# Performance work log

Hardware: AMD Instinct MI355X
Metric: run time of the kernel (lower is better)

## Reference

```python
import jax, jax.numpy as jnp
import numpy as np
from jax import lax

B, H, W, C, NH = 16, 56, 56, 192, 6
L = H * W
DH = C // NH            # 32
HID = 4 * C             # 768
ETA = 1.0 / DH          # TTT inner-loop learning rate
EPS = 1e-5

# ---- RoPE rotation tables (deterministic buffer, shape (H, W, C//2)) ----
_kmax = C // 4
_theta = 1.0 / (10000.0 ** (np.arange(_kmax) / _kmax))
_ii, _jj = np.meshgrid(np.arange(H), np.arange(W), indexing='ij')
_ang = np.concatenate([_ii[..., None] * _theta, _jj[..., None] * _theta], axis=-1)  # (H,W,C/2)
_COS = jnp.asarray(np.cos(_ang), dtype=jnp.float32)
_SIN = jnp.asarray(np.sin(_ang), dtype=jnp.float32)


def layernorm(x, g, b):
    mu = jnp.mean(x, axis=-1, keepdims=True)
    var = jnp.mean(jnp.square(x - mu), axis=-1, keepdims=True)
    return (x - mu) * lax.rsqrt(var + EPS) * g + b


def dwconv3x3(x_blc, w, b):
    # x: (B, L, Ch) -> depthwise 3x3 conv over (H, W) -> (B, L, Ch)
    Ch = x_blc.shape[-1]
    xi = x_blc.reshape(B, H, W, Ch).transpose(0, 3, 1, 2)  # NCHW
    y = lax.conv_general_dilated(xi, w, (1, 1), 'SAME', feature_group_count=Ch,
                                 dimension_numbers=('NCHW', 'OIHW', 'NCHW'))
    y = y + b[None, :, None, None]
    return y.transpose(0, 2, 3, 1).reshape(B, L, Ch)


def rope(x):
    # x: (B, L, C); rotate complex pairs with 2D axial angles
    xr = x.reshape(B, H, W, C // 2, 2)
    re, im = xr[..., 0], xr[..., 1]
    o_re = _COS * re - _SIN * im
    o_im = _SIN * re + _COS * im
    return jnp.stack([o_re, o_im], axis=-1).reshape(B, L, C)


def ttt_attn(xn, qkv_w, qkv_b, W0, proj_w, proj_b):
    qkv = xn @ qkv_w.T + qkv_b                      # (B, L, 3C)
    q, k, v = jnp.split(qkv, 3, axis=-1)
    q = rope(q) * (DH ** -0.5)
    k = rope(k)

    def to_heads(t):  # (B,L,C) -> (L, B*NH, DH)
        return t.reshape(B, L, NH, DH).transpose(1, 0, 2, 3).reshape(L, B * NH, DH)
    qs, ks, vs = to_heads(q), to_heads(k), to_heads(v)

    Wst0 = jnp.broadcast_to(W0[None], (B, NH, DH, DH)).reshape(B * NH, DH, DH)

    def step(Wst, qkv_t):
        qt, kt, vt = qkv_t
        pred = jnp.einsum('bij,bj->bi', Wst, kt)
        Wn = Wst - ETA * (pred - vt)[:, :, None] * kt[:, None, :]
        ot = jnp.einsum('bij,bj->bi', Wn, qt)
        return Wn, ot

    _, out = lax.scan(step, Wst0, (qs, ks, vs))     # out: (L, B*NH, DH)
    out = out.reshape(L, B, NH, DH).transpose(1, 0, 2, 3).reshape(B, L, C)
    return out @ proj_w.T + proj_b


def setup_inputs() -> dict:
    key = jax.random.key(0)
    ks = jax.random.split(key, 12)
    s = 0.02
    return {
        'x': jax.random.normal(ks[0], (B, L, C), jnp.float32),
        'cpe_w': jax.random.normal(ks[1], (C, 1, 3, 3), jnp.float32) * s,
        'cpe_b': jnp.zeros((C,), jnp.float32),
        'n1_g': jnp.ones((C,), jnp.float32),
        'n1_b': jnp.zeros((C,), jnp.float32),
        'qkv_w': jax.random.normal(ks[2], (3 * C, C), jnp.float32) * s,
        'qkv_b': jnp.zeros((3 * C,), jnp.float32),
        'W0': jax.random.normal(ks[3], (NH, DH, DH), jnp.float32) * s,
        'proj_w': jax.random.normal(ks[4], (C, C), jnp.float32) * s,
        'proj_b': jnp.zeros((C,), jnp.float32),
        'n2_g': jnp.ones((C,), jnp.float32),
        'n2_b': jnp.zeros((C,), jnp.float32),
        'fc1_w': jax.random.normal(ks[5], (HID, C), jnp.float32) * s,
        'fc1_b': jnp.zeros((HID,), jnp.float32),
        'dwc_w': jax.random.normal(ks[6], (HID, 1, 3, 3), jnp.float32) * s,
        'dwc_b': jnp.zeros((HID,), jnp.float32),
        'fc2_w': jax.random.normal(ks[7], (C, HID), jnp.float32) * s,
        'fc2_b': jnp.zeros((C,), jnp.float32),
    }


def reference(x, cpe_w, cpe_b, n1_g, n1_b, qkv_w, qkv_b, W0, proj_w, proj_b,
              n2_g, n2_b, fc1_w, fc1_b, dwc_w, dwc_b, fc2_w, fc2_b):
    # CPE: conditional positional encoding (depthwise conv residual)
    x = x + dwconv3x3(x, cpe_w, cpe_b)
    # TTT attention branch
    x = x + ttt_attn(layernorm(x, n1_g, n1_b), qkv_w, qkv_b, W0, proj_w, proj_b)
    # MLP branch with depthwise conv
    h1 = jax.nn.gelu(layernorm(x, n2_g, n2_b) @ fc1_w.T + fc1_b, approximate=False)
    h1 = jax.nn.gelu(h1 + dwconv3x3(h1, dwc_w, dwc_b), approximate=False)
    x = x + (h1 @ fc2_w.T + fc2_b)
    return x
```

## Files before the change

### kernel.cpp

```cpp
#include <hip/hip_runtime.h>
#include <hip/hip_bf16.h>

#define Bc 16
#define Hc 56
#define Wcc 56
#define Cc 192
#define NHc 6
#define Lc 3136
#define DHc 32
#define HIDc 768
#define NHEAD 96
#define Sc 32
#define NCHUNK 98
#define NPAIR (NHEAD*NCHUNK)
#define ROWS (Bc*Lc)
#define GR2 (ROWS/2)
#define ETAc (1.0f/32.0f)

typedef unsigned short u16;
typedef unsigned int u32;
typedef __attribute__((ext_vector_type(8))) short bf16x8;
typedef __attribute__((ext_vector_type(4))) float f32x4;
typedef __attribute__((ext_vector_type(16))) float f32x16;

__device__ __forceinline__ float b2f(u16 v){ u32 u = ((u32)v)<<16; float f; __builtin_memcpy(&f,&u,4); return f; }
__device__ __forceinline__ u16 f2b(float f){ u32 u; __builtin_memcpy(&u,&f,4); u32 r = u + 0x7FFFu + ((u>>16)&1u); return (u16)(r>>16); }
__device__ __forceinline__ f32x16 zero16(){ f32x16 z = {0,0,0,0,0,0,0,0,0,0,0,0,0,0,0,0}; return z; }

__device__ __forceinline__ void make_bfrags(const f32x16& t, int hi, bf16x8& b1, bf16x8& b2){
  u32 P[8], S[8];
  #pragma unroll
  for (int q=0;q<4;q++){
    #pragma unroll
    for (int j=0;j<2;j++){
      u32 r; float lo = t[4*q+2*j], hv = t[4*q+2*j+1];
      asm("v_cvt_pk_bf16_f32 %0, %1, %2" : "=v"(r) : "v"(lo), "v"(hv));
      P[2*q+j] = r;
    }
  }
  #pragma unroll
  for (int i=0;i<8;i++) S[i] = (u32)__shfl_xor((int)P[i], 32);
  union { u32 u[4]; bf16x8 v; } f1, f2;
  if (hi==0){ f1.u[0]=P[0]; f1.u[1]=P[1]; f1.u[2]=S[0]; f1.u[3]=S[1];
              f2.u[0]=P[4]; f2.u[1]=P[5]; f2.u[2]=S[4]; f2.u[3]=S[5]; }
  else      { f1.u[0]=S[2]; f1.u[1]=S[3]; f1.u[2]=P[2]; f1.u[3]=P[3];
              f2.u[0]=S[6]; f2.u[1]=S[7]; f2.u[2]=P[6]; f2.u[3]=P[7]; }
  b1 = f1.v; b2 = f2.v;
}

__global__ __launch_bounds__(256) void prep_kernel(
    const float* __restrict__ qkvw, const float* __restrict__ projw,
    const float* __restrict__ fc1w, const float* __restrict__ fc2w,
    const float* __restrict__ dwcw, const float* __restrict__ cpew,
    u16* __restrict__ wbqkv, u16* __restrict__ wbproj, u16* __restrict__ wbfc1,
    u16* __restrict__ wbfc2, float* __restrict__ dwt9, float* __restrict__ cwt9){
  int i = blockIdx.x*256 + threadIdx.x;
  if (i < 110592) wbqkv[i] = f2b(qkvw[i]);
  else if (i < 147456){ int j=i-110592; wbproj[j] = f2b(projw[j]); }
  else if (i < 294912){ int j=i-147456; wbfc1[j] = f2b(fc1w[j]); }
  else if (i < 442368){ int j=i-294912; wbfc2[j] = f2b(fc2w[j]); }
  else if (i < 449280){ int j=i-442368; int ch=j/9, t=j-ch*9; dwt9[t*HIDc+ch] = dwcw[j]; }
  else if (i < 451008){ int j=i-449280; int ch=j/9, t=j-ch*9; cwt9[t*Cc+ch] = cpew[j]; }
}

__global__ __launch_bounds__(256) void rope_tab_kernel(float* __restrict__ ct, float* __restrict__ st){
  int i = blockIdx.x*256 + threadIdx.x;
  int l = i/96, p = i - l*96;
  int h = l/Wcc, w = l - h*Wcc;
  int kk = (p<48)? p : p-48;
  float th = powf(10000.f, -(float)kk/48.f);
  float ang = (float)((p<48)? h : w) * th;
  ct[i] = cosf(ang);
  st[i] = sinf(ang);
}

__global__ __launch_bounds__(192) void cpe_ln_kernel(const float* __restrict__ x, const float* __restrict__ cwt9,
                                                     const float* __restrict__ bs, const float* __restrict__ g,
                                                     const float* __restrict__ b,
                                                     u16* __restrict__ x1, u16* __restrict__ xn){
  __shared__ float ps[192], pq[192], smu[8], srs[8];
  int tid = threadIdx.x;
  int rl = tid/24, sub = tid - rl*24, ch0 = sub*8;
  int row = blockIdx.x*8 + rl;
  int l = row % Lc; int h = l/Wcc, w = l - h*Wcc;
  const float* xp = x + (size_t)row*Cc + ch0;
  float acc[8];
  { f32x4 b0 = *(const f32x4*)(bs+ch0), b1v = *(const f32x4*)(bs+ch0+4);
    acc[0]=b0[0];acc[1]=b0[1];acc[2]=b0[2];acc[3]=b0[3];
    acc[4]=b1v[0];acc[5]=b1v[1];acc[6]=b1v[2];acc[7]=b1v[3]; }
  #pragma unroll
  for (int kh=0;kh<3;kh++){
    int hh = h+kh-1; if (hh<0 || hh>=Hc) continue;
    #pragma unroll
    for (int kw=0;kw<3;kw++){
      int ww = w+kw-1; if (ww<0 || ww>=Wcc) continue;
      const float* ip = xp + ((kh-1)*Wcc + (kw-1))*Cc;
      f32x4 i0 = *(const f32x4*)ip, i1 = *(const f32x4*)(ip+4);
      const float* wp = cwt9 + (kh*3+kw)*Cc + ch0;
      f32x4 w0 = *(const f32x4*)wp, w1 = *(const f32x4*)(wp+4);
      acc[0] += i0[0]*w0[0]; acc[1] += i0[1]*w0[1]; acc[2] += i0[2]*w0[2]; acc[3] += i0[3]*w0[3];
      acc[4] += i1[0]*w1[0]; acc[5] += i1[1]*w1[1]; acc[6] += i1[2]*w1[2]; acc[7] += i1[3]*w1[3];
    }
  }
  float val[8];
  { f32x4 c0 = *(const f32x4*)xp, c1 = *(const f32x4*)(xp+4);
    val[0]=c0[0]+acc[0]; val[1]=c0[1]+acc[1]; val[2]=c0[2]+acc[2]; val[3]=c0[3]+acc[3];
    val[4]=c1[0]+acc[4]; val[5]=c1[1]+acc[5]; val[6]=c1[2]+acc[6]; val[7]=c1[3]+acc[7]; }
  float s8=0.f, q8=0.f;
  #pragma unroll
  for (int j=0;j<8;j++){ s8 += val[j]; q8 += val[j]*val[j]; }
  ps[tid]=s8; pq[tid]=q8;
  __syncthreads();
  if (tid < 8){
    float s=0.f, q=0.f;
    #pragma unroll
    for (int k=0;k<24;k++){ s += ps[tid*24+k]; q += pq[tid*24+k]; }
    float mu = s*(1.f/Cc);
    float var = q*(1.f/Cc) - mu*mu;
    smu[tid] = mu; srs[tid] = rsqrtf(var + 1e-5f);
  }
  __syncthreads();
  float mu = smu[rl], rstd = srs[rl];
  union { bf16x8 v; u16 s[8]; } o1, o2;
  f32x4 g0 = *(const f32x4*)(g+ch0), g1 = *(const f32x4*)(g+ch0+4);
  f32x4 bb0 = *(const f32x4*)(b+ch0), bb1 = *(const f32x4*)(b+ch0+4);
  float gg[8] = {g0[0],g0[1],g0[2],g0[3],g1[0],g1[1],g1[2],g1[3]};
  float bbv[8] = {bb0[0],bb0[1],bb0[2],bb0[3],bb1[0],bb1[1],bb1[2],bb1[3]};
  #pragma unroll
  for (int j=0;j<8;j++){
    o1.s[j] = f2b(val[j]);
    o2.s[j] = f2b((val[j]-mu)*rstd*gg[j] + bbv[j]);
  }
  *(bf16x8*)(x1 + (size_t)row*Cc + ch0) = o1.v;
  *(bf16x8*)(xn + (size_t)row*Cc + ch0) = o2.v;
}

__global__ __launch_bounds__(256) void ln_kernel(const u16* __restrict__ xb, const float* __restrict__ g,
                                                 const float* __restrict__ b, u16* __restrict__ out){
  int row = blockIdx.x*4 + (threadIdx.x>>6);
  int lane = threadIdx.x & 63;
  const u16* xr = xb + (size_t)row*Cc;
  float v0 = b2f(xr[lane]), v1 = b2f(xr[lane+64]), v2 = b2f(xr[lane+128]);
  float s = v0+v1+v2;
  float q = v0*v0 + v1*v1 + v2*v2;
  #pragma unroll
  for (int off=32; off; off>>=1){ s += __shfl_xor(s, off); q += __shfl_xor(q, off); }
  float mu = s*(1.f/Cc);
  float var = q*(1.f/Cc) - mu*mu;
  float rstd = rsqrtf(var + 1e-5f);
  u16* orow = out + (size_t)row*Cc;
  orow[lane]     = f2b((v0-mu)*rstd*g[lane]     + b[lane]);
  orow[lane+64]  = f2b((v1-mu)*rstd*g[lane+64]  + b[lane+64]);
  orow[lane+128] = f2b((v2-mu)*rstd*g[lane+128] + b[lane+128]);
}

template<int MODE, int NB, int KT>
__global__ __launch_bounds__(256) void gemm_kernel(
    const u16* __restrict__ A, const u16* __restrict__ Wt,
    const float* __restrict__ bias,
    float* __restrict__ outf, u16* __restrict__ outb, u16* __restrict__ vdst,
    const u16* __restrict__ residb,
    const float* __restrict__ ct, const float* __restrict__ st,
    u16* __restrict__ q_s, u16* __restrict__ k_s)
{
  constexpr int NCH = KT/192;
  __shared__ __align__(16) u16 As[64*200];
  __shared__ __align__(16) u16 Osu[64*200];
  float* Os32 = (float*)Osu;
  int tid = threadIdx.x;
  int wid = tid>>6, lane = tid&63;
  int wr = wid>>1, wc = wid&1;
  int m0 = blockIdx.x*64;
  int ar = lane&15, kg = lane>>4;

  if constexpr (NCH == 1){
    #pragma unroll
    for (int j=0;j<6;j++){
      int g = j*256 + tid;
      int grow = g/24, gcol = (g - grow*24)*8;
      *(bf16x8*)(As + grow*200 + gcol) = *(const bf16x8*)(A + (size_t)(m0+grow)*192 + gcol);
    }
    __syncthreads();
    #pragma unroll
    for (int nb=0; nb<NB; nb++){
      const int nblk = nb*192;
      const int n0 = nblk + wc*96;
      f32x4 acc[2][6];
      #pragma unroll
      for (int f=0;f<2;f++)
        #pragma unroll
        for (int c=0;c<6;c++){ f32x4 z={0.f,0.f,0.f,0.f}; acc[f][c]=z; }
      bf16x8 bcur[6], bnxt[6];
      #pragma unroll
      for (int c=0;c<6;c++) bcur[c] = *(const bf16x8*)(Wt + (size_t)(n0 + c*16 + ar)*192 + kg*8);
      #pragma unroll
      for (int kc=0;kc<6;kc++){
        if (kc < 5){
          #pragma unroll
          for (int c=0;c<6;c++) bnxt[c] = *(const bf16x8*)(Wt + (size_t)(n0 + c*16 + ar)*192 + (kc+1)*32 + kg*8);
        }
        bf16x8 af[2];
        #pragma unroll
        for (int f=0;f<2;f++)
          af[f] = *(const bf16x8*)(As + (wr*32 + f*16 + ar)*200 + kc*32 + kg*8);
        #pragma unroll
        for (int f=0;f<2;f++)
          #pragma unroll
          for (int c=0;c<6;c++)
            acc[f][c] = __builtin_amdgcn_mfma_f32_16x16x32_bf16(af[f], bcur[c], acc[f][c], 0,0,0);
        #pragma unroll
        for (int c=0;c<6;c++) bcur[c] = bnxt[c];
      }
      __syncthreads();
      #pragma unroll
      for (int f=0;f<2;f++){
        #pragma unroll
        for (int c=0;c<6;c++){
          float bv = bias[n0 + c*16 + ar];
          #pragma unroll
          for (int j=0;j<4;j++){
            float v = acc[f][c][j] + bv;
            if (MODE==2) v = 0.5f*v*(1.f + erff(v*0.70710678118654752f));
            Osu[(wr*32 + f*16 + kg*4 + j)*200 + wc*96 + c*16 + ar] = f2b(v);
          }
        }
      }
      __syncthreads();
      #pragma unroll
      for (int j=0;j<6;j++){
        int g = j*256 + tid;
        int grow = g/24, gcol = (g - grow*24)*8;
        bf16x8 v = *(const bf16x8*)(Osu + grow*200 + gcol);
        int row = m0 + grow;
        if (MODE==2){
          *(bf16x8*)(outb + (size_t)row*HIDc + nblk + gcol) = v;
        } else if (MODE==1){
          bf16x8 rv = *(const bf16x8*)(residb + (size_t)row*Cc + gcol);
          union { bf16x8 v; u16 s[8]; } o;
          #pragma unroll
          for (int t=0;t<8;t++) o.s[t] = f2b(b2f((u16)v[t]) + b2f((u16)rv[t]));
          *(bf16x8*)(outb + (size_t)row*Cc + gcol) = o.v;
        } else {
          int bb = row/Lc; int l = row - bb*Lc;
          int nh = gcol>>5, d = gcol&31;
          if (nb < 2){
            const bool isq = (nb == 0);
            int p0 = gcol>>1;
            f32x4 cv = *(const f32x4*)(ct + l*96 + p0);
            f32x4 sv = *(const f32x4*)(st + l*96 + p0);
            float sc = isq ? 0.1767766952966369f : 1.0f;
            union { bf16x8 v; u16 s[8]; } o;
            #pragma unroll
            for (int t=0;t<4;t++){
              float re = b2f((u16)v[2*t]), im = b2f((u16)v[2*t+1]);
              o.s[2*t]   = f2b((cv[t]*re - sv[t]*im)*sc);
              o.s[2*t+1] = f2b((sv[t]*re + cv[t]*im)*sc);
            }
            u16* dst = (isq ? q_s : k_s) + (((size_t)(bb*NHc+nh))*Lc + l)*DHc + d;
            *(bf16x8*)dst = o.v;
          } else {
            *(bf16x8*)(vdst + (((size_t)(bb*NHc+nh))*Lc + l)*DHc + d) = v;
          }
        }
      }
    }
  } else {
    const int n0 = wc*96;
    f32x4 acc[2][6];
    #pragma unroll
    for (int f=0;f<2;f++)
      #pragma unroll
      for (int c=0;c<6;c++){ f32x4 z={0.f,0.f,0.f,0.f}; acc[f][c]=z; }
    bf16x8 bcur[6], bnxt[6];
    #pragma unroll
    for (int c=0;c<6;c++) bcur[c] = *(const bf16x8*)(Wt + (size_t)(n0 + c*16 + ar)*KT + kg*8);
    #pragma unroll
    for (int ch=0; ch<NCH; ch++){
      if (ch>0) __syncthreads();
      #pragma unroll
      for (int j=0;j<6;j++){
        int g = j*256 + tid;
        int grow = g/24, gcol = (g - grow*24)*8;
        *(bf16x8*)(As + grow*200 + gcol) = *(const bf16x8*)(A + (size_t)(m0+grow)*KT + ch*192 + gcol);
      }
      __syncthreads();
      #pragma unroll
      for (int kc=0;kc<6;kc++){
        int s = ch*6 + kc;
        if (s+1 < NCH*6){
          int koff = ((s+1)/6)*192 + ((s+1)%6)*32 + kg*8;
          #pragma unroll
          for (int c=0;c<6;c++) bnxt[c] = *(const bf16x8*)(Wt + (size_t)(n0 + c*16 + ar)*KT + koff);
        }
        bf16x8 af[2];
        #pragma unroll
        for (int f=0;f<2;f++)
          af[f] = *(const bf16x8*)(As + (wr*32 + f*16 + ar)*200 + kc*32 + kg*8);
        #pragma unroll
        for (int f=0;f<2;f++)
          #pragma unroll
          for (int c=0;c<6;c++)
            acc[f][c] = __builtin_amdgcn_mfma_f32_16x16x32_bf16(af[f], bcur[c], acc[f][c], 0,0,0);
        #pragma unroll
        for (int c=0;c<6;c++) bcur[c] = bnxt[c];
      }
    }
    #pragma unroll
    for (int half=0; half<2; half++){
      __syncthreads();
      if (wc==half){
        #pragma unroll
        for (int f=0;f<2;f++){
          #pragma unroll
          for (int c=0;c<6;c++){
            float bv = bias[n0 + c*16 + ar];
            #pragma unroll
            for (int j=0;j<4;j++)
              Os32[(wr*32 + f*16 + kg*4 + j)*100 + c*16 + ar] = acc[f][c][j] + bv;
          }
        }
      }
      __syncthreads();
      #pragma unroll
      for (int j=0;j<6;j++){
        int g = j*256 + tid;
        int grow = g/24, qcol = (g - grow*24)*4;
        f32x4 v = *(const f32x4*)(Os32 + grow*100 + qcol);
        int row = m0 + grow, colg = half*96 + qcol;
        const u16* rp = residb + (size_t)row*Cc + colg;
        v[0] += b2f(rp[0]); v[1] += b2f(rp[1]); v[2] += b2f(rp[2]); v[3] += b2f(rp[3]);
        *(f32x4*)(outf + (size_t)row*Cc + colg) = v;
      }
    }
  }
}

__global__ __launch_bounds__(256) void dwc_kernel(const u16* __restrict__ h1, const float* __restrict__ wt9,
                                                  const float* __restrict__ bs, u16* __restrict__ h2, int row0){
  int gid = blockIdx.x*256 + threadIdx.x;
  int cg = gid % 96; int lrow = gid / 96; int ch0 = cg*8;
  int row = row0 + lrow;
  int l = row % Lc; int h = l/Wcc, w = l - h*Wcc;
  const u16* hp = h1 + (size_t)lrow*HIDc + ch0;
  float acc[8];
  { f32x4 b0 = *(const f32x4*)(bs+ch0), b1v = *(const f32x4*)(bs+ch0+4);
    acc[0]=b0[0];acc[1]=b0[1];acc[2]=b0[2];acc[3]=b0[3];
    acc[4]=b1v[0];acc[5]=b1v[1];acc[6]=b1v[2];acc[7]=b1v[3]; }
  #pragma unroll
  for (int kh=0;kh<3;kh++){
    int hh = h+kh-1; if (hh<0 || hh>=Hc) continue;
    #pragma unroll
    for (int kw=0;kw<3;kw++){
      int ww = w+kw-1; if (ww<0 || ww>=Wcc) continue;
      bf16x8 iv = *(const bf16x8*)(hp + ((kh-1)*Wcc + (kw-1))*HIDc);
      const float* wp = wt9 + (kh*3+kw)*HIDc + ch0;
      f32x4 w0 = *(const f32x4*)wp, w1 = *(const f32x4*)(wp+4);
      acc[0] += b2f((u16)iv[0])*w0[0]; acc[1] += b2f((u16)iv[1])*w0[1];
      acc[2] += b2f((u16)iv[2])*w0[2]; acc[3] += b2f((u16)iv[3])*w0[3];
      acc[4] += b2f((u16)iv[4])*w1[0]; acc[5] += b2f((u16)iv[5])*w1[1];
      acc[6] += b2f((u16)iv[6])*w1[2]; acc[7] += b2f((u16)iv[7])*w1[3];
    }
  }
  bf16x8 cv = *(const bf16x8*)hp;
  union { bf16x8 v; u16 s[8]; } ov;
  #pragma unroll
  for (int j=0;j<8;j++){
    float v = b2f((u16)cv[j]) + acc[j];
    ov.s[j] = f2b(0.5f*v*(1.f + erff(v*0.70710678118654752f)));
  }
  *(bf16x8*)(h2 + (size_t)lrow*HIDc + ch0) = ov.v;
}

__global__ __launch_bounds__(64) void ttta_kernel(const u16* __restrict__ k_s, const u16* __restrict__ v_s,
                                                  u16* __restrict__ u_s, u16* __restrict__ rn_s,
                                                  u16* __restrict__ af_s, u16* __restrict__ bc_s){
  __shared__ float Gl[1024];
  __shared__ u16 LK[32*40];
  __shared__ float LU[32*33];
  __shared__ float LR[32*33];
  int pair = blockIdx.x;
  int head = pair / NCHUNK;
  int l0 = (pair - head*NCHUNK) * Sc;
  int lane = threadIdx.x; int rr = lane&31; int hi = lane>>5; int ks = hi*8;
  const u16* kb = k_s + ((size_t)head*Lc + l0)*DHc;
  bf16x8 a0 = *(const bf16x8*)(kb + rr*32 + ks);
  bf16x8 a1 = *(const bf16x8*)(kb + rr*32 + 16 + ks);
  *(bf16x8*)(LK + rr*40 + ks) = a0;
  *(bf16x8*)(LK + rr*40 + 16 + ks) = a1;
  f32x16 g = zero16();
  g = __builtin_amdgcn_mfma_f32_32x32x16_bf16(a0, a0, g, 0,0,0);
  g = __builtin_amdgcn_mfma_f32_32x32x16_bf16(a1, a1, g, 0,0,0);
  #pragma unroll
  for (int reg=0;reg<16;reg++){
    int i = (reg&3) + 8*(reg>>2) + 4*hi;
    Gl[i*32 + rr] = ETAc * g[reg];
  }
  __syncthreads();
  float X[32];
  if (lane < 32){
    #pragma unroll
    for (int i=0;i<32;i++) X[i] = ETAc * b2f(v_s[((size_t)head*Lc + l0 + i)*DHc + lane]);
  } else {
    int m = lane-32;
    #pragma unroll
    for (int i=0;i<32;i++) X[i] = ETAc * b2f(kb[i*32 + m]);
  }
  #pragma unroll
  for (int i=1;i<32;i++){
    float a = X[i];
    #pragma unroll
    for (int j=0;j<i;j++) a -= Gl[i*32+j]*X[j];
    X[i] = a;
  }
  if (lane < 32){
    u16* dst = u_s + (size_t)pair*1024 + lane;
    #pragma unroll
    for (int i=0;i<32;i++) dst[i*32] = f2b(X[i]);
    #pragma unroll
    for (int i=0;i<32;i++) LU[lane*33 + i] = X[i];
  } else {
    u16* dst = rn_s + (size_t)pair*1024 + (lane&31);
    #pragma unroll
    for (int i=0;i<32;i++) dst[i*32] = f2b(-X[i]);
    #pragma unroll
    for (int i=0;i<32;i++) LR[(lane&31)*33 + i] = X[i];
  }
  __syncthreads();
  union { bf16x8 v; u16 s[8]; } kc1, kc2, uc1, uc2, rc1, rc2;
  #pragma unroll
  for (int s=0;s<8;s++){
    kc1.s[s] = LK[(ks+s)*40 + rr];
    kc2.s[s] = LK[(16+ks+s)*40 + rr];
    uc1.s[s] = f2b(LU[rr*33 + ks+s]);
    uc2.s[s] = f2b(LU[rr*33 + 16+ks+s]);
    rc1.s[s] = f2b(LR[rr*33 + ks+s]);
    rc2.s[s] = f2b(LR[rr*33 + 16+ks+s]);
  }
  f32x16 bacc = zero16();
  bacc = __builtin_amdgcn_mfma_f32_32x32x16_bf16(kc1.v, uc1.v, bacc, 0,0,0);
  bacc = __builtin_amdgcn_mfma_f32_32x32x16_bf16(kc2.v, uc2.v, bacc, 0,0,0);
  union { bf16x8 v; u16 s[8]; } bo1, bo2;
  #pragma unroll
  for (int r=0;r<8;r++){ bo1.s[r] = f2b(bacc[r]); bo2.s[r] = f2b(bacc[8+r]); }
  *(bf16x8*)(bc_s + (size_t)pair*1024 + lane*16) = bo1.v;
  *(bf16x8*)(bc_s + (size_t)pair*1024 + lane*16 + 8) = bo2.v;
  f32x16 aacc = zero16();
  aacc = __builtin_amdgcn_mfma_f32_32x32x16_bf16(rc1.v, kc1.v, aacc, 0,0,0);
  aacc = __builtin_amdgcn_mfma_f32_32x32x16_bf16(rc2.v, kc2.v, aacc, 0,0,0);
  f32x16 an;
  #pragma unroll
  for (int r=0;r<16;r++) an[r] = -aacc[r];
  bf16x8 f1, f2;
  make_bfrags(an, hi, f1, f2);
  *(bf16x8*)(af_s + (size_t)pair*1024 + lane*16) = f1;
  *(bf16x8*)(af_s + (size_t)pair*1024 + lane*16 + 8) = f2;
}

__global__ __launch_bounds__(64) void tttb_kernel(const u16* __restrict__ af_s, const u16* __restrict__ bc_s,
                                                  const float* __restrict__ W0, u16* __restrict__ w_snap){
  int head = blockIdx.x; int nh = head % NHc;
  int lane = threadIdx.x; int rr = lane&31; int hi = lane>>5;
  f32x16 T;
  const float* w0r = W0 + nh*1024 + rr*32 + 4*hi;
  #pragma unroll
  for (int q=0;q<4;q++){
    f32x4 v = *(const f32x4*)(w0r + 8*q);
    T[4*q+0]=v[0]; T[4*q+1]=v[1]; T[4*q+2]=v[2]; T[4*q+3]=v[3];
  }
  size_t hb = (size_t)head*NCHUNK;
  const bf16x8* afp = (const bf16x8*)(af_s + hb*1024);
  const bf16x8* bcp = (const bf16x8*)(bc_s + hb*1024);
  bf16x8 A1 = afp[lane*2], A2 = afp[lane*2+1];
  bf16x8 Bv1 = bcp[lane*2], Bv2 = bcp[lane*2+1];
  bf16x8 b1, b2;
  make_bfrags(T, hi, b1, b2);
  for (int c=0;c<NCHUNK;c++){
    bf16x8 nA1=A1, nA2=A2, nB1=Bv1, nB2=Bv2;
    if (c+1 < NCHUNK){
      int base = (c+1)*128 + lane*2;
      nA1 = afp[base]; nA2 = afp[base+1];
      nB1 = bcp[base]; nB2 = bcp[base+1];
    }
    u16* wrow = w_snap + (hb + c)*1024 + rr*32;
    *(bf16x8*)(wrow + hi*8) = b1;
    *(bf16x8*)(wrow + 16 + hi*8) = b2;
    f32x16 acc;
    #pragma unroll
    for (int r=0;r<8;r++){ acc[r] = T[r] + b2f((u16)Bv1[r]); acc[8+r] = T[8+r] + b2f((u16)Bv2[r]); }
    acc = __builtin_amdgcn_mfma_f32_32x32x16_bf16(A1, b1, acc, 0,0,0);
    acc = __builtin_amdgcn_mfma_f32_32x32x16_bf16(A2, b2, acc, 0,0,0);
    T = acc;
    make_bfrags(T, hi, b1, b2);
    A1=nA1; A2=nA2; Bv1=nB1; Bv2=nB2;
  }
}

__global__ __launch_bounds__(64) void tttc_kernel(const u16* __restrict__ q_s, const u16* __restrict__ k_s,
                                                  const u16* __restrict__ w_snap, const u16* __restrict__ u_s,
                                                  const u16* __restrict__ rn_s, u16* __restrict__ o_bf){
  __shared__ __align__(16) u16 Pl[32*40];
  int pair = blockIdx.x;
  int head = pair / NCHUNK;
  int ch = pair - head*NCHUNK;
  int l0 = ch*Sc;
  int lane = threadIdx.x; int rr = lane&31; int hi = lane>>5; int ks = hi*8;
  const u16* qb = q_s + ((size_t)head*Lc + l0)*DHc;
  const u16* kb = k_s + ((size_t)head*Lc + l0)*DHc;
  bf16x8 q0 = *(const bf16x8*)(qb + rr*32 + ks);
  bf16x8 q1 = *(const bf16x8*)(qb + rr*32 + 16 + ks);
  bf16x8 k0 = *(const bf16x8*)(kb + rr*32 + ks);
  bf16x8 k1 = *(const bf16x8*)(kb + rr*32 + 16 + ks);
  f32x16 p = zero16();
  p = __builtin_amdgcn_mfma_f32_32x32x16_bf16(q0, k0, p, 0,0,0);
  p = __builtin_amdgcn_mfma_f32_32x32x16_bf16(q1, k1, p, 0,0,0);
  #pragma unroll
  for (int reg=0;reg<16;reg++){
    int i = (reg&3)+8*(reg>>2)+4*hi;
    Pl[i*40+rr] = (rr<=i) ? f2b(p[reg]) : (u16)0;
  }
  const u16* wsb = w_snap + (size_t)pair*1024;
  bf16x8 tb0 = *(const bf16x8*)(wsb + rr*32 + ks);
  bf16x8 tb1 = *(const bf16x8*)(wsb + rr*32 + 16 + ks);
  const u16* ub = u_s + (size_t)pair*1024;
  f32x16 wr;
  #pragma unroll
  for (int r=0;r<16;r++){
    int i = (r&3)+8*(r>>2)+4*hi;
    wr[r] = b2f(ub[i*32 + rr]);
  }
  const u16* rb = rn_s + (size_t)pair*1024;
  bf16x8 rn0 = *(const bf16x8*)(rb + rr*32 + ks);
  bf16x8 rn1 = *(const bf16x8*)(rb + rr*32 + 16 + ks);
  wr = __builtin_amdgcn_mfma_f32_32x32x16_bf16(rn0, tb0, wr, 0,0,0);
  wr = __builtin_amdgcn_mfma_f32_32x32x16_bf16(rn1, tb1, wr, 0,0,0);
  bf16x8 wb0, wb1;
  make_bfrags(wr, hi, wb0, wb1);
  __syncthreads();
  f32x16 o = zero16();
  o = __builtin_amdgcn_mfma_f32_32x32x16_bf16(q0, tb0, o, 0,0,0);
  o = __builtin_amdgcn_mfma_f32_32x32x16_bf16(q1, tb1, o, 0,0,0);
  bf16x8 pa0 = *(const bf16x8*)(Pl + rr*40 + ks);
  bf16x8 pa1 = *(const bf16x8*)(Pl + rr*40 + 16 + ks);
  o = __builtin_amdgcn_mfma_f32_32x32x16_bf16(pa0, wb0, o, 0,0,0);
  o = __builtin_amdgcn_mfma_f32_32x32x16_bf16(pa1, wb1, o, 0,0,0);
  int bb = head/NHc, nh = head - bb*NHc;
  #pragma unroll
  for (int reg=0;reg<16;reg++){
    int i = (reg&3)+8*(reg>>2)+4*hi;
    o_bf[((size_t)(bb*Lc + l0 + i))*Cc + nh*32 + rr] = f2b(o[reg]);
  }
}

extern "C" void kernel_launch(void* const* d_in, const int* in_sizes, int n_in,
                              void* d_out, int out_size, void* d_ws, size_t ws_size,
                              hipStream_t stream){
  const float* x     = (const float*)d_in[0];
  const float* cpe_w = (const float*)d_in[1];
  const float* cpe_b = (const float*)d_in[2];
  const float* n1_g  = (const float*)d_in[3];
  const float* n1_b  = (const float*)d_in[4];
  const float* qkv_w = (const float*)d_in[5];
  const float* qkv_b = (const float*)d_in[6];
  const float* W0    = (const float*)d_in[7];
  const float* proj_w= (const float*)d_in[8];
  const float* proj_b= (const float*)d_in[9];
  const float* n2_g  = (const float*)d_in[10];
  const float* n2_b  = (const float*)d_in[11];
  const float* fc1_w = (const float*)d_in[12];
  const float* fc1_b = (const float*)d_in[13];
  const float* dwc_w = (const float*)d_in[14];
  const float* dwc_b = (const float*)d_in[15];
  const float* fc2_w = (const float*)d_in[16];
  const float* fc2_b = (const float*)d_in[17];

  char* ws = (char*)d_ws;
  size_t off = 0;
  auto alloc = [&](size_t bytes)->char*{
    char* p = ws + off;
    off += (bytes + 255) & ~(size_t)255;
    return p;
  };
  u16* wbqkv = (u16*)alloc((size_t)576*192*2);
  u16* wbproj= (u16*)alloc((size_t)192*192*2);
  u16* wbfc1 = (u16*)alloc((size_t)768*192*2);
  u16* wbfc2 = (u16*)alloc((size_t)192*768*2);
  float* dwt9 = (float*)alloc((size_t)9*HIDc*4);
  float* cwt9 = (float*)alloc((size_t)9*Cc*4);
  float* ctab = (float*)alloc((size_t)Lc*96*4);
  float* stab = (float*)alloc((size_t)Lc*96*4);
  u16* regA = (u16*)alloc((size_t)ROWS*Cc*2);
  u16* regB = (u16*)alloc((size_t)ROWS*Cc*2);
  u16* regC = (u16*)alloc((size_t)NHEAD*Lc*DHc*2);
  u16* regD = (u16*)alloc((size_t)NHEAD*Lc*DHc*2);
  u16* regE = (u16*)alloc((size_t)NHEAD*Lc*DHc*2);
  u16* rn_s = (u16*)alloc((size_t)NPAIR*1024*2);
  u16* af_s = (u16*)alloc((size_t)NPAIR*1024*2);
  u16* us = (u16*)d_out;
  u16* bc = us + (size_t)NPAIR*1024;

  u16* x1 = regA;
  u16* x2b = regA;
  u16* xn = regB;
  u16* obf = regB;
  u16* xn2 = regB;
  u16* qs = regC;
  u16* vs = regD;
  u16* wsn = regD;
  u16* ksb = regE;
  u16* h1 = regD;
  u16* h2 = rn_s;

  prep_kernel<<<(451008+255)/256,256,0,stream>>>(qkv_w, proj_w, fc1_w, fc2_w, dwc_w, cpe_w,
                                                 wbqkv, wbproj, wbfc1, wbfc2, dwt9, cwt9);
  rope_tab_kernel<<<(Lc*96)/256,256,0,stream>>>(ctab, stab);

  cpe_ln_kernel<<<ROWS/8,192,0,stream>>>(x, cwt9, cpe_b, n1_g, n1_b, x1, xn);
  gemm_kernel<0,3,192><<<ROWS/64,256,0,stream>>>(xn, wbqkv, qkv_b,
      nullptr, nullptr, vs, nullptr, ctab, stab, qs, ksb);
  ttta_kernel<<<NPAIR,64,0,stream>>>(ksb, vs, us, rn_s, af_s, bc);
  tttb_kernel<<<NHEAD,64,0,stream>>>(af_s, bc, W0, wsn);
  tttc_kernel<<<NPAIR,64,0,stream>>>(qs, ksb, wsn, us, rn_s, obf);
  gemm_kernel<1,1,192><<<ROWS/64,256,0,stream>>>(obf, wbproj, proj_b,
      nullptr, x2b, nullptr, x1, nullptr, nullptr, nullptr, nullptr);
  ln_kernel<<<ROWS/4,256,0,stream>>>(x2b, n2_g, n2_b, xn2);
  for (int g4=0; g4<2; g4++){
    const u16* a_in = xn2 + (size_t)g4*GR2*Cc;
    float* xo = (float*)d_out + (size_t)g4*GR2*Cc;
    const u16* res = x2b + (size_t)g4*GR2*Cc;
    gemm_kernel<2,4,192><<<GR2/64,256,0,stream>>>(a_in, wbfc1, fc1_b,
        nullptr, h1, nullptr, nullptr, nullptr, nullptr, nullptr, nullptr);
    dwc_kernel<<<(GR2*96)/256,256,0,stream>>>(h1, dwt9, dwc_b, h2, g4*GR2);
    gemm_kernel<3,1,768><<<GR2/64,256,0,stream>>>(h2, wbfc2, fc2_b,
        xo, nullptr, nullptr, res, nullptr, nullptr, nullptr, nullptr);
  }
}
```

Baseline: 513.3 us.

## Fuse LayerNorm into proj GEMM epilogue and recompute TTT chunk solves in tttc

```diff
diff --git a/kernel.cpp b/kernel.cpp
--- a/kernel.cpp
+++ b/kernel.cpp
@@ -135,25 +135,6 @@
   *(bf16x8*)(xn + (size_t)row*Cc + ch0) = o2.v;
 }
 
-__global__ __launch_bounds__(256) void ln_kernel(const u16* __restrict__ xb, const float* __restrict__ g,
-                                                 const float* __restrict__ b, u16* __restrict__ out){
-  int row = blockIdx.x*4 + (threadIdx.x>>6);
-  int lane = threadIdx.x & 63;
-  const u16* xr = xb + (size_t)row*Cc;
-  float v0 = b2f(xr[lane]), v1 = b2f(xr[lane+64]), v2 = b2f(xr[lane+128]);
-  float s = v0+v1+v2;
-  float q = v0*v0 + v1*v1 + v2*v2;
-  #pragma unroll
-  for (int off=32; off; off>>=1){ s += __shfl_xor(s, off); q += __shfl_xor(q, off); }
-  float mu = s*(1.f/Cc);
-  float var = q*(1.f/Cc) - mu*mu;
-  float rstd = rsqrtf(var + 1e-5f);
-  u16* orow = out + (size_t)row*Cc;
-  orow[lane]     = f2b((v0-mu)*rstd*g[lane]     + b[lane]);
-  orow[lane+64]  = f2b((v1-mu)*rstd*g[lane+64]  + b[lane+64]);
-  orow[lane+128] = f2b((v2-mu)*rstd*g[lane+128] + b[lane+128]);
-}
-
 template<int MODE, int NB, int KT>
 __global__ __launch_bounds__(256) void gemm_kernel(
     const u16* __restrict__ A, const u16* __restrict__ Wt,
@@ -161,7 +142,8 @@
     float* __restrict__ outf, u16* __restrict__ outb, u16* __restrict__ vdst,
     const u16* __restrict__ residb,
     const float* __restrict__ ct, const float* __restrict__ st,
-    u16* __restrict__ q_s, u16* __restrict__ k_s)
+    u16* __restrict__ q_s, u16* __restrict__ k_s,
+    const float* __restrict__ lng, const float* __restrict__ lnb, u16* __restrict__ xnout)
 {
   constexpr int NCH = KT/192;
   __shared__ __align__(16) u16 As[64*200];
@@ -240,6 +222,7 @@
           #pragma unroll
           for (int t=0;t<8;t++) o.s[t] = f2b(b2f((u16)v[t]) + b2f((u16)rv[t]));
           *(bf16x8*)(outb + (size_t)row*Cc + gcol) = o.v;
+          *(bf16x8*)(Osu + grow*200 + gcol) = o.v;
         } else {
           int bb = row/Lc; int l = row - bb*Lc;
           int nh = gcol>>5, d = gcol&31;
@@ -264,6 +247,29 @@
         }
       }
     }
+    if (MODE==1){
+      __syncthreads();
+      int rowl = tid>>2, q = tid&3;
+      const u16* orow = Osu + rowl*200 + q*48;
+      float s=0.f, qq=0.f;
+      #pragma unroll
+      for (int c=0;c<48;c++){ float v = b2f(orow[c]); s += v; qq += v*v; }
+      s += __shfl_xor(s,1); qq += __shfl_xor(qq,1);
+      s += __shfl_xor(s,2); qq += __shfl_xor(qq,2);
+      float mu = s*(1.f/192.f);
+      float rstd = rsqrtf(qq*(1.f/192.f) - mu*mu + 1e-5f);
+      int row = m0 + rowl;
+      #pragma unroll
+      for (int c8=0;c8<6;c8++){
+        union { bf16x8 v; u16 s[8]; } ox;
+        #pragma unroll
+        for (int t=0;t<8;t++){
+          int col = q*48 + c8*8 + t;
+          ox.s[t] = f2b((b2f(orow[c8*8+t])-mu)*rstd*lng[col] + lnb[col]);
+        }
+        *(bf16x8*)(xnout + (size_t)row*Cc + q*48 + c8*8) = ox.v;
+      }
+    }
   } else {
     const int n0 = wc*96;
     f32x4 acc[2][6];
@@ -372,7 +378,6 @@
 }
 
 __global__ __launch_bounds__(64) void ttta_kernel(const u16* __restrict__ k_s, const u16* __restrict__ v_s,
-                                                  u16* __restrict__ u_s, u16* __restrict__ rn_s,
                                                   u16* __restrict__ af_s, u16* __restrict__ bc_s){
   __shared__ float Gl[1024];
   __shared__ u16 LK[32*40];
@@ -413,15 +418,9 @@
     X[i] = a;
   }
   if (lane < 32){
-    u16* dst = u_s + (size_t)pair*1024 + lane;
-    #pragma unroll
-    for (int i=0;i<32;i++) dst[i*32] = f2b(X[i]);
     #pragma unroll
     for (int i=0;i<32;i++) LU[lane*33 + i] = X[i];
   } else {
-    u16* dst = rn_s + (size_t)pair*1024 + (lane&31);
-    #pragma unroll
-    for (int i=0;i<32;i++) dst[i*32] = f2b(-X[i]);
     #pragma unroll
     for (int i=0;i<32;i++) LR[(lane&31)*33 + i] = X[i];
   }
@@ -496,20 +495,56 @@
 }
 
 __global__ __launch_bounds__(64) void tttc_kernel(const u16* __restrict__ q_s, const u16* __restrict__ k_s,
-                                                  const u16* __restrict__ w_snap, const u16* __restrict__ u_s,
-                                                  const u16* __restrict__ rn_s, u16* __restrict__ o_bf){
+                                                  const u16* __restrict__ v_s, const u16* __restrict__ w_snap,
+                                                  u16* __restrict__ o_bf){
+  __shared__ float Gl[1024];
+  __shared__ float LU[32*33];
+  __shared__ float LR[32*33];
   __shared__ __align__(16) u16 Pl[32*40];
   int pair = blockIdx.x;
   int head = pair / NCHUNK;
   int ch = pair - head*NCHUNK;
   int l0 = ch*Sc;
   int lane = threadIdx.x; int rr = lane&31; int hi = lane>>5; int ks = hi*8;
+  const u16* kb = k_s + ((size_t)head*Lc + l0)*DHc;
   const u16* qb = q_s + ((size_t)head*Lc + l0)*DHc;
-  const u16* kb = k_s + ((size_t)head*Lc + l0)*DHc;
+  bf16x8 k0 = *(const bf16x8*)(kb + rr*32 + ks);
+  bf16x8 k1 = *(const bf16x8*)(kb + rr*32 + 16 + ks);
+  f32x16 g = zero16();
+  g = __builtin_amdgcn_mfma_f32_32x32x16_bf16(k0, k0, g, 0,0,0);
+  g = __builtin_amdgcn_mfma_f32_32x32x16_bf16(k1, k1, g, 0,0,0);
+  #pragma unroll
+  for (int reg=0;reg<16;reg++){
+    int i = (reg&3) + 8*(reg>>2) + 4*hi;
+    Gl[i*32 + rr] = ETAc * g[reg];
+  }
+  __syncthreads();
+  float X[32];
+  if (lane < 32){
+    #pragma unroll
+    for (int i=0;i<32;i++) X[i] = ETAc * b2f(v_s[((size_t)head*Lc + l0 + i)*DHc + lane]);
+  } else {
+    int m = lane-32;
+    #pragma unroll
+    for (int i=0;i<32;i++) X[i] = ETAc * b2f(kb[i*32 + m]);
+  }
+  #pragma unroll
+  for (int i=1;i<32;i++){
+    float a = X[i];
+    #pragma unroll
+    for (int j=0;j<i;j++) a -= Gl[i*32+j]*X[j];
+    X[i] = a;
+  }
+  if (lane < 32){
+    #pragma unroll
+    for (int i=0;i<32;i++) LU[lane*33 + i] = X[i];
+  } else {
+    #pragma unroll
+    for (int i=0;i<32;i++) LR[(lane&31)*33 + i] = X[i];
+  }
+  __syncthreads();
   bf16x8 q0 = *(const bf16x8*)(qb + rr*32 + ks);
   bf16x8 q1 = *(const bf16x8*)(qb + rr*32 + 16 + ks);
-  bf16x8 k0 = *(const bf16x8*)(kb + rr*32 + ks);
-  bf16x8 k1 = *(const bf16x8*)(kb + rr*32 + 16 + ks);
   f32x16 p = zero16();
   p = __builtin_amdgcn_mfma_f32_32x32x16_bf16(q0, k0, p, 0,0,0);
   p = __builtin_amdgcn_mfma_f32_32x32x16_bf16(q1, k1, p, 0,0,0);
@@ -521,18 +556,20 @@
   const u16* wsb = w_snap + (size_t)pair*1024;
   bf16x8 tb0 = *(const bf16x8*)(wsb + rr*32 + ks);
   bf16x8 tb1 = *(const bf16x8*)(wsb + rr*32 + 16 + ks);
-  const u16* ub = u_s + (size_t)pair*1024;
   f32x16 wr;
   #pragma unroll
   for (int r=0;r<16;r++){
     int i = (r&3)+8*(r>>2)+4*hi;
-    wr[r] = b2f(ub[i*32 + rr]);
-  }
-  const u16* rb = rn_s + (size_t)pair*1024;
-  bf16x8 rn0 = *(const bf16x8*)(rb + rr*32 + ks);
-  bf16x8 rn1 = *(const bf16x8*)(rb + rr*32 + 16 + ks);
-  wr = __builtin_amdgcn_mfma_f32_32x32x16_bf16(rn0, tb0, wr, 0,0,0);
-  wr = __builtin_amdgcn_mfma_f32_32x32x16_bf16(rn1, tb1, wr, 0,0,0);
+    wr[r] = LU[rr*33 + i];
+  }
+  union { bf16x8 v; u16 s[8]; } rn0, rn1;
+  #pragma unroll
+  for (int s=0;s<8;s++){
+    rn0.s[s] = f2b(-LR[(ks+s)*33 + rr]);
+    rn1.s[s] = f2b(-LR[(16+ks+s)*33 + rr]);
+  }
+  wr = __builtin_amdgcn_mfma_f32_32x32x16_bf16(rn0.v, tb0, wr, 0,0,0);
+  wr = __builtin_amdgcn_mfma_f32_32x32x16_bf16(rn1.v, tb1, wr, 0,0,0);
   bf16x8 wb0, wb1;
   make_bfrags(wr, hi, wb0, wb1);
   __syncthreads();
@@ -593,10 +630,9 @@
   u16* regC = (u16*)alloc((size_t)NHEAD*Lc*DHc*2);
   u16* regD = (u16*)alloc((size_t)NHEAD*Lc*DHc*2);
   u16* regE = (u16*)alloc((size_t)NHEAD*Lc*DHc*2);
-  u16* rn_s = (u16*)alloc((size_t)NPAIR*1024*2);
+  u16* regF = (u16*)alloc((size_t)NPAIR*1024*2);
   u16* af_s = (u16*)alloc((size_t)NPAIR*1024*2);
-  u16* us = (u16*)d_out;
-  u16* bc = us + (size_t)NPAIR*1024;
+  u16* bc = (u16*)d_out;
 
   u16* x1 = regA;
   u16* x2b = regA;
@@ -605,10 +641,10 @@
   u16* xn2 = regB;
   u16* qs = regC;
   u16* vs = regD;
-  u16* wsn = regD;
   u16* ksb = regE;
+  u16* wsn = regF;
   u16* h1 = regD;
-  u16* h2 = rn_s;
+  u16* h2 = regF;
 
   prep_kernel<<<(451008+255)/256,256,0,stream>>>(qkv_w, proj_w, fc1_w, fc2_w, dwc_w, cpe_w,
                                                  wbqkv, wbproj, wbfc1, wbfc2, dwt9, cwt9);
@@ -616,21 +652,20 @@
 
   cpe_ln_kernel<<<ROWS/8,192,0,stream>>>(x, cwt9, cpe_b, n1_g, n1_b, x1, xn);
   gemm_kernel<0,3,192><<<ROWS/64,256,0,stream>>>(xn, wbqkv, qkv_b,
-      nullptr, nullptr, vs, nullptr, ctab, stab, qs, ksb);
-  ttta_kernel<<<NPAIR,64,0,stream>>>(ksb, vs, us, rn_s, af_s, bc);
+      nullptr, nullptr, vs, nullptr, ctab, stab, qs, ksb, nullptr, nullptr, nullptr);
+  ttta_kernel<<<NPAIR,64,0,stream>>>(ksb, vs, af_s, bc);
   tttb_kernel<<<NHEAD,64,0,stream>>>(af_s, bc, W0, wsn);
-  tttc_kernel<<<NPAIR,64,0,stream>>>(qs, ksb, wsn, us, rn_s, obf);
+  tttc_kernel<<<NPAIR,64,0,stream>>>(qs, ksb, vs, wsn, obf);
   gemm_kernel<1,1,192><<<ROWS/64,256,0,stream>>>(obf, wbproj, proj_b,
-      nullptr, x2b, nullptr, x1, nullptr, nullptr, nullptr, nullptr);
-  ln_kernel<<<ROWS/4,256,0,stream>>>(x2b, n2_g, n2_b, xn2);
+      nullptr, x2b, nullptr, x1, nullptr, nullptr, nullptr, nullptr, n2_g, n2_b, xn2);
   for (int g4=0; g4<2; g4++){
     const u16* a_in = xn2 + (size_t)g4*GR2*Cc;
     float* xo = (float*)d_out + (size_t)g4*GR2*Cc;
     const u16* res = x2b + (size_t)g4*GR2*Cc;
     gemm_kernel<2,4,192><<<GR2/64,256,0,stream>>>(a_in, wbfc1, fc1_b,
-        nullptr, h1, nullptr, nullptr, nullptr, nullptr, nullptr, nullptr);
+        nullptr, h1, nullptr, nullptr, nullptr, nullptr, nullptr, nullptr, nullptr, nullptr, nullptr);
     dwc_kernel<<<(GR2*96)/256,256,0,stream>>>(h1, dwt9, dwc_b, h2, g4*GR2);
     gemm_kernel<3,1,768><<<GR2/64,256,0,stream>>>(h2, wbfc2, fc2_b,
-        xo, nullptr, nullptr, res, nullptr, nullptr, nullptr, nullptr);
-  }
-}
+        xo, nullptr, nullptr, res, nullptr, nullptr, nullptr, nullptr, nullptr, nullptr, nullptr);
+  }
+}
```

Result: no change. 520.2 us (+1.3%).
